# Kernel tuning notes

Hardware: AMD Instinct MI355X
Metric: run time of the kernel (lower is better)

Reference implementation:

```python
import jax, jax.numpy as jnp
import numpy as np


def setup_inputs() -> dict:
    key = jax.random.key(0)
    k1, k2 = jax.random.split(key)
    N, D, C = 65536, 512, 64
    embeddings = jax.random.normal(k1, (N, D), dtype=jnp.float32)
    labels = jax.random.randint(k2, (N,), 0, C, dtype=jnp.int64)
    return {"embeddings": embeddings, "labels": labels, "num_classes": C}


def reference(embeddings, labels, num_classes):
    # Per-class mean (prototypes) via segment reductions. Labels are assumed
    # to be 0..C-1 with all classes present, so unique(labels) == arange(C)
    # and local_labels == labels (faithful to the torch loop in that regime).
    ones = jnp.ones(labels.shape, dtype=embeddings.dtype)
    counts = jax.ops.segment_sum(ones, labels, num_segments=num_classes)  # [C]
    sums = jax.ops.segment_sum(embeddings, labels, num_segments=num_classes)  # [C, D]
    prototypes = sums / counts[:, None]

    # Euclidean cdist: ||e||^2 + ||p||^2 - 2 e.p^T, clamped for numerical safety
    e2 = jnp.sum(embeddings * embeddings, axis=1, keepdims=True)  # [N, 1]
    p2 = jnp.sum(prototypes * prototypes, axis=1)  # [C]
    cross = embeddings @ prototypes.T  # [N, C]
    d2 = jnp.maximum(e2 + p2[None, :] - 2.0 * cross, 1e-12)
    logits = -jnp.sqrt(d2)  # [N, C], negative distances

    log_probs = jax.nn.log_softmax(logits, axis=1)
    n = labels.shape[0]
    nll = -log_probs[jnp.arange(n), labels]
    loss = jnp.mean(nll)
    accuracy = jnp.mean((jnp.argmax(logits, axis=1) == labels).astype(jnp.float32))
    return (loss, accuracy)
```

## Files before the change

kernel.cpp:

```cpp
#include <hip/hip_runtime.h>
#include <math.h>

#define NROWS 65536
#define DIM   512
#define NCLS  64
#define CCAP  1280

typedef __attribute__((ext_vector_type(4))) float f32x4;
typedef __attribute__((ext_vector_type(8))) short s16x8;

#define WS_PROTOSUM 0
#define WS_CURSORS  32768
#define WS_LOSS     32832
#define WS_ACC      32833
#define WS_DONE     32834
#define WS_P2       32836
#define WS_PERM     32912
#define WS_PB       32912
#define MEMSET_WORDS 32835

static __device__ __forceinline__ unsigned short f2bf(float f) {
    unsigned int u = __float_as_uint(f);
    u += 0x7FFF + ((u >> 16) & 1);
    return (unsigned short)(u >> 16);
}
static __device__ __forceinline__ float bf2f(unsigned short h) {
    return __uint_as_float(((unsigned int)h) << 16);
}

__global__ __launch_bounds__(256) void k_scatter(const int* __restrict__ labels,
                                                 int* __restrict__ cursors,
                                                 int* __restrict__ perm) {
    __shared__ int lh[NCLS], lb[NCLS];
    int t = threadIdx.x;
    if (t < NCLS) lh[t] = 0;
    __syncthreads();
    int i = blockIdx.x * 256 + t;
    int lab = labels[i];
    int rank = atomicAdd(&lh[lab], 1);
    __syncthreads();
    if (t < NCLS) lb[t] = atomicAdd(&cursors[t], lh[t]);
    __syncthreads();
    int pos = lb[lab] + rank;
    if (pos < CCAP) perm[lab * CCAP + pos] = i;
}

__global__ __launch_bounds__(256) void k_psum(const float* __restrict__ emb,
                                              const int* __restrict__ cursors,
                                              const int* __restrict__ perm,
                                              float* __restrict__ protoSum) {
    __shared__ int permS[CCAP];
    __shared__ float4 red[256];
    int t   = threadIdx.x;
    int c   = blockIdx.x >> 5;
    int sub = blockIdx.x & 31;
    int dc  = sub & 3;
    int rs  = sub >> 2;
    int tl  = t & 31;
    int g   = t >> 5;

    int cnt = cursors[c];
    int n = (cnt < CCAP) ? cnt : CCAP;
    for (int i = t; i < n; i += 256) permS[i] = perm[c * CCAP + i];
    __syncthreads();

    const float4* eb = (const float4*)emb + dc * 32 + tl;
    float4 acc = make_float4(0.f, 0.f, 0.f, 0.f);
#pragma unroll 4
    for (int i = rs * 8 + g; i < n; i += 64) {
        int r = permS[i];
        float4 v = eb[(size_t)r * 128];
        acc.x += v.x; acc.y += v.y; acc.z += v.z; acc.w += v.w;
    }
    red[t] = acc;
    __syncthreads();
    if (t < 32) {
        float4 s = red[t];
#pragma unroll
        for (int gg = 1; gg < 8; ++gg) {
            float4 v = red[gg * 32 + t];
            s.x += v.x; s.y += v.y; s.z += v.z; s.w += v.w;
        }
        float* dst = &protoSum[(size_t)c * DIM + dc * 128 + t * 4];
        atomicAdd(dst + 0, s.x);
        atomicAdd(dst + 1, s.y);
        atomicAdd(dst + 2, s.z);
        atomicAdd(dst + 3, s.w);
    }
}

__global__ __launch_bounds__(512) void k_protofin(const float* __restrict__ protoSum,
                                                  const int* __restrict__ cursors,
                                                  unsigned short* __restrict__ pB,
                                                  float* __restrict__ p2) {
    int c = blockIdx.x, d = threadIdx.x;
    float mean = protoSum[(size_t)c * DIM + d] / (float)cursors[c];
    unsigned short mb = f2bf(mean);
    pB[(size_t)c * DIM + d] = mb;
    float mf = bf2f(mb);
    float sq = mf * mf;
#pragma unroll
    for (int o = 32; o > 0; o >>= 1) sq += __shfl_down(sq, o, 64);
    __shared__ float red[8];
    if ((d & 63) == 0) red[d >> 6] = sq;
    __syncthreads();
    if (d == 0) {
        float ss = 0.f;
#pragma unroll
        for (int w = 0; w < 8; ++w) ss += red[w];
        p2[c] = ss;
    }
}

#define LROWS 64
#define LGRID (NROWS / LROWS)
__global__ __launch_bounds__(256) void k_logits(const float* __restrict__ emb,
                                                const int* __restrict__ labels,
                                                const unsigned short* __restrict__ pB,
                                                const float* __restrict__ p2,
                                                float* __restrict__ lossAcc,
                                                float* __restrict__ accAcc,
                                                unsigned int* __restrict__ doneCnt,
                                                float* __restrict__ out) {
    __shared__ float e2s[LROWS];
    __shared__ float rb[8];

    int t    = threadIdx.x;
    int lane = t & 63;
    int wv   = t >> 6;
    int quad = lane >> 4;
    int l15  = lane & 15;
    int rbase = blockIdx.x * LROWS;

    f32x4 acc[4];
#pragma unroll
    for (int nt = 0; nt < 4; ++nt) acc[nt] = (f32x4){0.f, 0.f, 0.f, 0.f};
    float e2a = 0.f;

    const float4* arow = (const float4*)(emb + (size_t)(rbase + wv * 16 + l15) * DIM)
                         + quad * 2;
    const unsigned short* bbase = pB + (size_t)l15 * DIM + quad * 8;

    for (int kc = 0; kc < 16; ++kc) {
        float4 a0 = arow[kc * 8 + 0];
        float4 a1 = arow[kc * 8 + 1];
        s16x8 bf[4];
#pragma unroll
        for (int nt = 0; nt < 4; ++nt)
            bf[nt] = *(const s16x8*)(bbase + (size_t)nt * 16 * DIM + kc * 32);
        e2a += a0.x * a0.x + a0.y * a0.y + a0.z * a0.z + a0.w * a0.w;
        e2a += a1.x * a1.x + a1.y * a1.y + a1.z * a1.z + a1.w * a1.w;
        s16x8 af;
        af[0] = (short)f2bf(a0.x); af[1] = (short)f2bf(a0.y);
        af[2] = (short)f2bf(a0.z); af[3] = (short)f2bf(a0.w);
        af[4] = (short)f2bf(a1.x); af[5] = (short)f2bf(a1.y);
        af[6] = (short)f2bf(a1.z); af[7] = (short)f2bf(a1.w);
#pragma unroll
        for (int nt = 0; nt < 4; ++nt)
            acc[nt] = __builtin_amdgcn_mfma_f32_16x16x32_bf16(af, bf[nt], acc[nt], 0, 0, 0);
    }

    e2a += __shfl_xor(e2a, 16, 64);
    e2a += __shfl_xor(e2a, 32, 64);
    if (lane < 16) e2s[wv * 16 + lane] = e2a;
    __syncthreads();

    float nlls = 0.f, corr = 0.f;
#pragma unroll
    for (int reg = 0; reg < 4; ++reg) {
        int rloc = wv * 16 + quad * 4 + reg;
        float e2v = e2s[rloc];
        float lg[4];
#pragma unroll
        for (int nt = 0; nt < 4; ++nt) {
            float d2 = e2v + p2[nt * 16 + l15] - 2.f * acc[nt][reg];
            d2 = fmaxf(d2, 1e-12f);
            lg[nt] = -sqrtf(d2);
        }
        float mv = lg[0]; int mc = l15;
#pragma unroll
        for (int nt = 1; nt < 4; ++nt) {
            int cix = nt * 16 + l15;
            if (lg[nt] > mv) { mv = lg[nt]; mc = cix; }
        }
#pragma unroll
        for (int o = 1; o < 16; o <<= 1) {
            float mo = __shfl_xor(mv, o, 64);
            int   co = __shfl_xor(mc, o, 64);
            if (mo > mv || (mo == mv && co < mc)) { mv = mo; mc = co; }
        }
        int lab = labels[rbase + rloc];
        float se = 0.f, ll = 0.f;
#pragma unroll
        for (int nt = 0; nt < 4; ++nt) se += __expf(lg[nt] - mv);
        if ((lab & 15) == l15) ll = lg[lab >> 4];
#pragma unroll
        for (int o = 1; o < 16; o <<= 1) {
            se += __shfl_xor(se, o, 64);
            ll += __shfl_xor(ll, o, 64);
        }
        if (l15 == 0) {
            nlls += __logf(se) + mv - ll;
            corr += (mc == lab) ? 1.f : 0.f;
        }
    }
#pragma unroll
    for (int o = 1; o < 64; o <<= 1) {
        nlls += __shfl_xor(nlls, o, 64);
        corr += __shfl_xor(corr, o, 64);
    }
    if (lane == 0) { rb[wv] = nlls; rb[4 + wv] = corr; }
    __syncthreads();
    if (t == 0) {
        atomicAdd(lossAcc, rb[0] + rb[1] + rb[2] + rb[3]);
        atomicAdd(accAcc, rb[4] + rb[5] + rb[6] + rb[7]);
        __threadfence();
        unsigned int tk = atomicAdd(doneCnt, 1u);
        if (tk == LGRID - 1) {
            float ls = atomicAdd(lossAcc, 0.f);
            float as_ = atomicAdd(accAcc, 0.f);
            out[0] = ls * (1.f / NROWS);
            out[1] = as_ * (1.f / NROWS);
        }
    }
}

extern "C" void kernel_launch(void* const* d_in, const int* in_sizes, int n_in,
                              void* d_out, int out_size, void* d_ws, size_t ws_size,
                              hipStream_t stream) {
    const float* emb    = (const float*)d_in[0];
    const int*   labels = (const int*)d_in[1];
    float* out = (float*)d_out;

    float* wsf = (float*)d_ws;
    int*   wsi = (int*)d_ws;
    float*          protoSum = wsf + WS_PROTOSUM;
    int*            cursors  = wsi + WS_CURSORS;
    float*          lossAcc  = wsf + WS_LOSS;
    float*          accAcc   = wsf + WS_ACC;
    unsigned int*   doneCnt  = (unsigned int*)(wsi + WS_DONE);
    float*          p2       = wsf + WS_P2;
    int*            perm     = wsi + WS_PERM;
    unsigned short* pB       = (unsigned short*)(wsf + WS_PB);

    hipMemsetAsync(d_ws, 0, MEMSET_WORDS * sizeof(int), stream);

    k_scatter<<<NROWS / 256, 256, 0, stream>>>(labels, cursors, perm);
    k_psum<<<NCLS * 32, 256, 0, stream>>>(emb, cursors, perm, protoSum);
    k_protofin<<<NCLS, 512, 0, stream>>>(protoSum, cursors, pB, p2);
    k_logits<<<LGRID, 256, 0, stream>>>(emb, labels, pB, p2,
                                        lossAcc, accAcc, doneCnt, out);
}
```

Baseline: 309.3 us.

## Stage embedding tiles through LDS with coalesced loads and prefetch; pre-swizzle prototype fragments

The logits kernel now loads embedding rows cooperatively with coalesced float4 reads, converts them to bf16, and stages them in a double-buffered LDS tile. MFMA A-fragments are read from that tile, and the next k-chunk is prefetched into registers. Prototypes are written by k_protofin in fragment order so each lane's B load is contiguous, and the workspace slot moves so pBf no longer aliases perm. The aim is better global-load coalescing and overlap of memory with compute, at the cost of one barrier per k-step and extra LDS use.

```diff
diff --git a/kernel.cpp b/kernel.cpp
--- a/kernel.cpp
+++ b/kernel.cpp
@@ -16,7 +16,7 @@
 #define WS_DONE     32834
 #define WS_P2       32836
 #define WS_PERM     32912
-#define WS_PB       32912
+#define WS_PBF      114944
 #define MEMSET_WORDS 32835
 
 static __device__ __forceinline__ unsigned short f2bf(float f) {
@@ -91,12 +91,14 @@
 
 __global__ __launch_bounds__(512) void k_protofin(const float* __restrict__ protoSum,
                                                   const int* __restrict__ cursors,
-                                                  unsigned short* __restrict__ pB,
+                                                  unsigned short* __restrict__ pBf,
                                                   float* __restrict__ p2) {
     int c = blockIdx.x, d = threadIdx.x;
     float mean = protoSum[(size_t)c * DIM + d] / (float)cursors[c];
     unsigned short mb = f2bf(mean);
-    pB[(size_t)c * DIM + d] = mb;
+    int kc = d >> 5, quad = (d >> 3) & 3, j = d & 7;
+    int nt = c >> 4, l15 = c & 15;
+    pBf[(size_t)(((kc * 4 + quad) * 4 + nt) * 16 + l15) * 8 + j] = mb;
     float mf = bf2f(mb);
     float sq = mf * mf;
 #pragma unroll
@@ -116,12 +118,13 @@
 #define LGRID (NROWS / LROWS)
 __global__ __launch_bounds__(256) void k_logits(const float* __restrict__ emb,
                                                 const int* __restrict__ labels,
-                                                const unsigned short* __restrict__ pB,
+                                                const unsigned short* __restrict__ pBf,
                                                 const float* __restrict__ p2,
                                                 float* __restrict__ lossAcc,
                                                 float* __restrict__ accAcc,
                                                 unsigned int* __restrict__ doneCnt,
                                                 float* __restrict__ out) {
+    __shared__ __align__(16) unsigned short Asm[2][LROWS * 36];
     __shared__ float e2s[LROWS];
     __shared__ float rb[8];
 
@@ -135,34 +138,60 @@
     f32x4 acc[4];
 #pragma unroll
     for (int nt = 0; nt < 4; ++nt) acc[nt] = (f32x4){0.f, 0.f, 0.f, 0.f};
-    float e2a = 0.f;
-
-    const float4* arow = (const float4*)(emb + (size_t)(rbase + wv * 16 + l15) * DIM)
-                         + quad * 2;
-    const unsigned short* bbase = pB + (size_t)l15 * DIM + quad * 8;
-
+    float e2a0 = 0.f, e2a1 = 0.f;
+
+    const float4* emb4 = (const float4*)(emb + (size_t)rbase * DIM);
+    int row0 = t >> 3, j0 = t & 7;
+    int row1 = 32 + row0;
+
+    float4 g0 = emb4[(size_t)row0 * 128 + j0];
+    float4 g1 = emb4[(size_t)row1 * 128 + j0];
+    s16x8 bf[4];
+#pragma unroll
+    for (int nt = 0; nt < 4; ++nt)
+        bf[nt] = *(const s16x8*)(pBf + (size_t)((quad * 4 + nt) * 16 + l15) * 8);
+
+#pragma unroll 4
     for (int kc = 0; kc < 16; ++kc) {
-        float4 a0 = arow[kc * 8 + 0];
-        float4 a1 = arow[kc * 8 + 1];
-        s16x8 bf[4];
+        int buf = kc & 1;
+        e2a0 += g0.x * g0.x + g0.y * g0.y + g0.z * g0.z + g0.w * g0.w;
+        e2a1 += g1.x * g1.x + g1.y * g1.y + g1.z * g1.z + g1.w * g1.w;
+        ushort4 h0, h1;
+        h0.x = f2bf(g0.x); h0.y = f2bf(g0.y); h0.z = f2bf(g0.z); h0.w = f2bf(g0.w);
+        h1.x = f2bf(g1.x); h1.y = f2bf(g1.y); h1.z = f2bf(g1.z); h1.w = f2bf(g1.w);
+        *(ushort4*)&Asm[buf][row0 * 36 + j0 * 4] = h0;
+        *(ushort4*)&Asm[buf][row1 * 36 + j0 * 4] = h1;
+
+        float4 n0, n1; s16x8 nb[4];
+        if (kc < 15) {
+            n0 = emb4[(size_t)row0 * 128 + (kc + 1) * 8 + j0];
+            n1 = emb4[(size_t)row1 * 128 + (kc + 1) * 8 + j0];
+#pragma unroll
+            for (int nt = 0; nt < 4; ++nt)
+                nb[nt] = *(const s16x8*)(pBf +
+                    (size_t)((((kc + 1) * 4 + quad) * 4 + nt) * 16 + l15) * 8);
+        }
+
+        asm volatile("s_waitcnt lgkmcnt(0)\n\ts_barrier" ::: "memory");
+
+        s16x8 a = *(const s16x8*)&Asm[buf][(wv * 16 + l15) * 36 + quad * 8];
 #pragma unroll
         for (int nt = 0; nt < 4; ++nt)
-            bf[nt] = *(const s16x8*)(bbase + (size_t)nt * 16 * DIM + kc * 32);
-        e2a += a0.x * a0.x + a0.y * a0.y + a0.z * a0.z + a0.w * a0.w;
-        e2a += a1.x * a1.x + a1.y * a1.y + a1.z * a1.z + a1.w * a1.w;
-        s16x8 af;
-        af[0] = (short)f2bf(a0.x); af[1] = (short)f2bf(a0.y);
-        af[2] = (short)f2bf(a0.z); af[3] = (short)f2bf(a0.w);
-        af[4] = (short)f2bf(a1.x); af[5] = (short)f2bf(a1.y);
-        af[6] = (short)f2bf(a1.z); af[7] = (short)f2bf(a1.w);
-#pragma unroll
-        for (int nt = 0; nt < 4; ++nt)
-            acc[nt] = __builtin_amdgcn_mfma_f32_16x16x32_bf16(af, bf[nt], acc[nt], 0, 0, 0);
-    }
-
-    e2a += __shfl_xor(e2a, 16, 64);
-    e2a += __shfl_xor(e2a, 32, 64);
-    if (lane < 16) e2s[wv * 16 + lane] = e2a;
+            acc[nt] = __builtin_amdgcn_mfma_f32_16x16x32_bf16(a, bf[nt], acc[nt], 0, 0, 0);
+
+        g0 = n0; g1 = n1;
+#pragma unroll
+        for (int nt = 0; nt < 4; ++nt) bf[nt] = nb[nt];
+    }
+
+    float v0 = e2a0;
+    v0 += __shfl_xor(v0, 1, 64); v0 += __shfl_xor(v0, 2, 64); v0 += __shfl_xor(v0, 4, 64);
+    float v1 = e2a1;
+    v1 += __shfl_xor(v1, 1, 64); v1 += __shfl_xor(v1, 2, 64); v1 += __shfl_xor(v1, 4, 64);
+    if ((lane & 7) == 0) {
+        e2s[wv * 8 + (lane >> 3)]      = v0;
+        e2s[32 + wv * 8 + (lane >> 3)] = v1;
+    }
     __syncthreads();
 
     float nlls = 0.f, corr = 0.f;
@@ -217,7 +246,7 @@
         __threadfence();
         unsigned int tk = atomicAdd(doneCnt, 1u);
         if (tk == LGRID - 1) {
-            float ls = atomicAdd(lossAcc, 0.f);
+            float ls  = atomicAdd(lossAcc, 0.f);
             float as_ = atomicAdd(accAcc, 0.f);
             out[0] = ls * (1.f / NROWS);
             out[1] = as_ * (1.f / NROWS);
@@ -241,13 +270,13 @@
     unsigned int*   doneCnt  = (unsigned int*)(wsi + WS_DONE);
     float*          p2       = wsf + WS_P2;
     int*            perm     = wsi + WS_PERM;
-    unsigned short* pB       = (unsigned short*)(wsf + WS_PB);
+    unsigned short* pBf      = (unsigned short*)(wsf + WS_PBF);
 
     hipMemsetAsync(d_ws, 0, MEMSET_WORDS * sizeof(int), stream);
 
     k_scatter<<<NROWS / 256, 256, 0, stream>>>(labels, cursors, perm);
     k_psum<<<NCLS * 32, 256, 0, stream>>>(emb, cursors, perm, protoSum);
-    k_protofin<<<NCLS, 512, 0, stream>>>(protoSum, cursors, pB, p2);
-    k_logits<<<LGRID, 256, 0, stream>>>(emb, labels, pB, p2,
+    k_protofin<<<NCLS, 512, 0, stream>>>(protoSum, cursors, pBf, p2);
+    k_logits<<<LGRID, 256, 0, stream>>>(emb, labels, pBf, p2,
                                         lossAcc, accAcc, doneCnt, out);
 }
```

After: 270.8 us. -12.4%, faster.

## Pipeline embedding loads into LDS via async DMA and prelayout prototype fragments

Applied to the files above, without the earlier changes.

The logits kernel now streams embedding rows into a triple-buffered, XOR-swizzled LDS ring using global_load_lds DMA, with explicit vmcnt waits. Prototype bf16 fragments are double-buffered in registers from a new fragment-ordered layout written by protofin. The e2 shared buffer and its barrier are replaced by wave shuffles, p2 is hoisted into registers, and the psum loop unroll is raised. The intent is to keep more memory loads in flight and hide HBM latency, at the cost of more LDS use and hand-tuned waitcnt correctness risk.

```diff
diff --git a/kernel.cpp b/kernel.cpp
--- a/kernel.cpp
+++ b/kernel.cpp
@@ -16,7 +16,7 @@
 #define WS_DONE     32834
 #define WS_P2       32836
 #define WS_PERM     32912
-#define WS_PB       32912
+#define WS_PBF      114944
 #define MEMSET_WORDS 32835
 
 static __device__ __forceinline__ unsigned short f2bf(float f) {
@@ -26,6 +26,12 @@
 }
 static __device__ __forceinline__ float bf2f(unsigned short h) {
     return __uint_as_float(((unsigned int)h) << 16);
+}
+
+static __device__ __forceinline__ void dma16(const void* g, const void* l) {
+    __builtin_amdgcn_global_load_lds(
+        (const __attribute__((address_space(1))) void*)g,
+        (__attribute__((address_space(3))) void*)l, 16, 0, 0);
 }
 
 __global__ __launch_bounds__(256) void k_scatter(const int* __restrict__ labels,
@@ -66,7 +72,7 @@
 
     const float4* eb = (const float4*)emb + dc * 32 + tl;
     float4 acc = make_float4(0.f, 0.f, 0.f, 0.f);
-#pragma unroll 4
+#pragma unroll 8
     for (int i = rs * 8 + g; i < n; i += 64) {
         int r = permS[i];
         float4 v = eb[(size_t)r * 128];
@@ -91,12 +97,14 @@
 
 __global__ __launch_bounds__(512) void k_protofin(const float* __restrict__ protoSum,
                                                   const int* __restrict__ cursors,
-                                                  unsigned short* __restrict__ pB,
+                                                  unsigned short* __restrict__ pBf,
                                                   float* __restrict__ p2) {
     int c = blockIdx.x, d = threadIdx.x;
     float mean = protoSum[(size_t)c * DIM + d] / (float)cursors[c];
     unsigned short mb = f2bf(mean);
-    pB[(size_t)c * DIM + d] = mb;
+    int kc = d >> 5, quad = (d >> 3) & 3, j = d & 7;
+    int nt = c >> 4, l15 = c & 15;
+    pBf[(size_t)(((kc * 4 + quad) * 4 + nt) * 16 + l15) * 8 + j] = mb;
     float mf = bf2f(mb);
     float sq = mf * mf;
 #pragma unroll
@@ -116,13 +124,13 @@
 #define LGRID (NROWS / LROWS)
 __global__ __launch_bounds__(256) void k_logits(const float* __restrict__ emb,
                                                 const int* __restrict__ labels,
-                                                const unsigned short* __restrict__ pB,
+                                                const unsigned short* __restrict__ pBf,
                                                 const float* __restrict__ p2,
                                                 float* __restrict__ lossAcc,
                                                 float* __restrict__ accAcc,
                                                 unsigned int* __restrict__ doneCnt,
                                                 float* __restrict__ out) {
-    __shared__ float e2s[LROWS];
+    __shared__ __align__(16) float Abuf[4][3][16][32];
     __shared__ float rb[8];
 
     int t    = threadIdx.x;
@@ -132,22 +140,47 @@
     int l15  = lane & 15;
     int rbase = blockIdx.x * LROWS;
 
+    int rw = lane >> 3;
+    int qs = lane & 7;
+    const float4* emb4 = (const float4*)emb;
+    size_t gbase = ((size_t)(rbase + wv * 16 + rw)) * 128 + (size_t)(qs ^ rw);
+    const char* lds0 = (const char*)&Abuf[wv][0][0][0];
+
     f32x4 acc[4];
 #pragma unroll
     for (int nt = 0; nt < 4; ++nt) acc[nt] = (f32x4){0.f, 0.f, 0.f, 0.f};
     float e2a = 0.f;
 
-    const float4* arow = (const float4*)(emb + (size_t)(rbase + wv * 16 + l15) * DIM)
-                         + quad * 2;
-    const unsigned short* bbase = pB + (size_t)l15 * DIM + quad * 8;
-
+    const float4* ar = (const float4*)lds0;
+
+    dma16(emb4 + gbase,        lds0);
+    dma16(emb4 + gbase + 1024, lds0 + 1024);
+    dma16(emb4 + gbase + 8,        lds0 + 2048);
+    dma16(emb4 + gbase + 1024 + 8, lds0 + 2048 + 1024);
+    s16x8 bfc[4], bfn[4];
+#pragma unroll
+    for (int nt = 0; nt < 4; ++nt)
+        bfc[nt] = *(const s16x8*)(pBf + (size_t)((quad * 4 + nt) * 16 + l15) * 8);
+
+#pragma unroll
     for (int kc = 0; kc < 16; ++kc) {
-        float4 a0 = arow[kc * 8 + 0];
-        float4 a1 = arow[kc * 8 + 1];
-        s16x8 bf[4];
-#pragma unroll
-        for (int nt = 0; nt < 4; ++nt)
-            bf[nt] = *(const s16x8*)(bbase + (size_t)nt * 16 * DIM + kc * 32);
+        const int b = kc % 3;
+        if (kc < 14) {
+            const int bn = (kc + 2) % 3;
+            dma16(emb4 + gbase + (kc + 2) * 8,        lds0 + bn * 2048);
+            dma16(emb4 + gbase + 1024 + (kc + 2) * 8, lds0 + bn * 2048 + 1024);
+        }
+        if (kc < 15) {
+#pragma unroll
+            for (int nt = 0; nt < 4; ++nt)
+                bfn[nt] = *(const s16x8*)(pBf +
+                    (size_t)((((kc + 1) * 4 + quad) * 4 + nt) * 16 + l15) * 8);
+        }
+        if (kc < 15) asm volatile("s_waitcnt vmcnt(8)" ::: "memory");
+        else         asm volatile("s_waitcnt vmcnt(0)" ::: "memory");
+
+        float4 a0 = ar[b * 128 + l15 * 8 + ((quad * 2)     ^ (l15 & 7))];
+        float4 a1 = ar[b * 128 + l15 * 8 + ((quad * 2 + 1) ^ (l15 & 7))];
         e2a += a0.x * a0.x + a0.y * a0.y + a0.z * a0.z + a0.w * a0.w;
         e2a += a1.x * a1.x + a1.y * a1.y + a1.z * a1.z + a1.w * a1.w;
         s16x8 af;
@@ -157,23 +190,27 @@
         af[6] = (short)f2bf(a1.z); af[7] = (short)f2bf(a1.w);
 #pragma unroll
         for (int nt = 0; nt < 4; ++nt)
-            acc[nt] = __builtin_amdgcn_mfma_f32_16x16x32_bf16(af, bf[nt], acc[nt], 0, 0, 0);
+            acc[nt] = __builtin_amdgcn_mfma_f32_16x16x32_bf16(af, bfc[nt], acc[nt], 0, 0, 0);
+#pragma unroll
+        for (int nt = 0; nt < 4; ++nt) bfc[nt] = bfn[nt];
     }
 
     e2a += __shfl_xor(e2a, 16, 64);
     e2a += __shfl_xor(e2a, 32, 64);
-    if (lane < 16) e2s[wv * 16 + lane] = e2a;
-    __syncthreads();
+
+    float p2r[4];
+#pragma unroll
+    for (int nt = 0; nt < 4; ++nt) p2r[nt] = p2[nt * 16 + l15];
 
     float nlls = 0.f, corr = 0.f;
 #pragma unroll
     for (int reg = 0; reg < 4; ++reg) {
         int rloc = wv * 16 + quad * 4 + reg;
-        float e2v = e2s[rloc];
+        float e2v = __shfl(e2a, quad * 4 + reg, 64);
         float lg[4];
 #pragma unroll
         for (int nt = 0; nt < 4; ++nt) {
-            float d2 = e2v + p2[nt * 16 + l15] - 2.f * acc[nt][reg];
+            float d2 = e2v + p2r[nt] - 2.f * acc[nt][reg];
             d2 = fmaxf(d2, 1e-12f);
             lg[nt] = -sqrtf(d2);
         }
@@ -217,7 +254,7 @@
         __threadfence();
         unsigned int tk = atomicAdd(doneCnt, 1u);
         if (tk == LGRID - 1) {
-            float ls = atomicAdd(lossAcc, 0.f);
+            float ls  = atomicAdd(lossAcc, 0.f);
             float as_ = atomicAdd(accAcc, 0.f);
             out[0] = ls * (1.f / NROWS);
             out[1] = as_ * (1.f / NROWS);
@@ -241,13 +278,13 @@
     unsigned int*   doneCnt  = (unsigned int*)(wsi + WS_DONE);
     float*          p2       = wsf + WS_P2;
     int*            perm     = wsi + WS_PERM;
-    unsigned short* pB       = (unsigned short*)(wsf + WS_PB);
+    unsigned short* pBf      = (unsigned short*)(wsf + WS_PBF);
 
     hipMemsetAsync(d_ws, 0, MEMSET_WORDS * sizeof(int), stream);
 
     k_scatter<<<NROWS / 256, 256, 0, stream>>>(labels, cursors, perm);
     k_psum<<<NCLS * 32, 256, 0, stream>>>(emb, cursors, perm, protoSum);
-    k_protofin<<<NCLS, 512, 0, stream>>>(protoSum, cursors, pB, p2);
-    k_logits<<<LGRID, 256, 0, stream>>>(emb, labels, pB, p2,
+    k_protofin<<<NCLS, 512, 0, stream>>>(protoSum, cursors, pBf, p2);
+    k_logits<<<LGRID, 256, 0, stream>>>(emb, labels, pBf, p2,
                                         lossAcc, accAcc, doneCnt, out);
 }
```

Result: faster. 274.6 us (-11.2%).
